# Kernel optimization log

Hardware: AMD Instinct MI355X
Metric: run time of the kernel (lower is better)

## Reference

```python
import jax, jax.numpy as jnp
import numpy as np
from jax import lax

B, T, U, V, D, H = 4, 256, 64, 1024, 256, 256
BLANK = V - 1
NEG = -1.0e30
CTC_W = 0.3


def setup_inputs():
    ks = jax.random.split(jax.random.key(0), 9)
    return {
        "x_enc": jax.random.normal(ks[0], (B, T, D), jnp.float32),
        "x_dec": jax.random.normal(ks[1], (B, U + 1, H), jnp.float32),
        "W_enc": jax.random.normal(ks[2], (D, H), jnp.float32) / float(np.sqrt(D)),
        "b_enc": jnp.zeros((H,), jnp.float32),
        "W_dec": jax.random.normal(ks[3], (H, H), jnp.float32) / float(np.sqrt(H)),
        "b_dec": jnp.zeros((H,), jnp.float32),
        "W_out": jax.random.normal(ks[4], (H, V), jnp.float32) / float(np.sqrt(H)),
        "b_out": jnp.zeros((V,), jnp.float32),
        "W_ctc": jax.random.normal(ks[5], (D, V), jnp.float32) / float(np.sqrt(D)),
        "b_ctc": jnp.zeros((V,), jnp.float32),
        "target": jax.random.randint(ks[6], (B, U), 0, V - 1, jnp.int32),
        "frame_length": (T - jax.random.randint(ks[7], (B,), 0, T // 4)).astype(jnp.int32),
        "target_length": (U - jax.random.randint(ks[8], (B,), 0, U // 4)).astype(jnp.int32),
    }


def _forward(x_enc, x_dec, W_enc, b_enc, W_dec, b_dec, W_out, b_out, W_ctc, b_ctc,
             target, frame_length, target_length):
    b_idx = jnp.arange(B)
    ft, tl = frame_length, target_length

    # ---- Joiner: broadcast-add of projected enc/pred states, tanh, output proj ----
    h = jnp.tanh((x_enc @ W_enc + b_enc)[:, :, None, :]
                 + (x_dec @ W_dec + b_dec)[:, None, :, :])        # [B,T,U+1,H]
    logp = jax.nn.log_softmax(h @ W_out + b_out, axis=-1)          # [B,T,U+1,V]

    # gather=True trick: only blank and target-label log-probs are needed
    lp_blank = logp[..., BLANK]                                    # [B,T,U+1]
    lp_label = jnp.take_along_axis(
        logp[:, :, :U, :],
        jnp.broadcast_to(target[:, None, :, None], (B, T, U, 1)), axis=3)[..., 0]  # [B,T,U]

    # ---- RNNT forward DP over the (T, U+1) lattice ----
    def u_scan(b0, lbl):
        # b0[u] = alpha[t-1,u] + blank[t-1,u]; alpha[t,u] = logaddexp(b0[u], alpha[t,u-1]+lbl[u-1])
        def step(c, xs):
            bu, lu = xs
            new = jnp.logaddexp(bu, c + lu)
            return new, new
        _, outs = lax.scan(step, b0[:, 0],
                           (jnp.moveaxis(b0[:, 1:], 1, 0), jnp.moveaxis(lbl, 1, 0)))
        return jnp.concatenate([b0[:, :1], jnp.moveaxis(outs, 0, 1)], axis=1)

    alpha0 = jnp.concatenate([jnp.zeros((B, 1), logp.dtype),
                              jnp.cumsum(lp_label[:, 0, :], axis=1)], axis=1)  # [B,U+1]

    def t_step(prev, xs):
        blk_prev, lbl_t = xs
        a = u_scan(prev + blk_prev, lbl_t)
        return a, a

    _, rest = lax.scan(t_step, alpha0,
                       (jnp.moveaxis(lp_blank[:, :-1, :], 1, 0),
                        jnp.moveaxis(lp_label[:, 1:, :], 1, 0)))
    alphas = jnp.concatenate([alpha0[None], rest], axis=0)          # [T,B,U+1]
    ll = alphas[ft - 1, b_idx, tl] + lp_blank[b_idx, ft - 1, tl]
    rnnt_loss = jnp.mean(-ll)

    # ---- CTC branch: linear head on encoder output + standard CTC DP ----
    logp_ctc = jax.nn.log_softmax(x_enc @ W_ctc + b_ctc, axis=-1)   # [B,T,V]
    S = 2 * U + 1
    ext = jnp.full((B, S), BLANK, jnp.int32).at[:, 1::2].set(target)
    emit = jnp.take_along_axis(logp_ctc,
                               jnp.broadcast_to(ext[:, None, :], (B, T, S)), axis=2)  # [B,T,S]
    skip = jnp.concatenate([jnp.zeros((B, 2), bool),
                            (ext[:, 2:] != BLANK) & (ext[:, 2:] != ext[:, :-2])], axis=1)
    c0 = jnp.full((B, S), NEG, logp_ctc.dtype).at[:, 0].set(emit[:, 0, 0]).at[:, 1].set(emit[:, 0, 1])

    def c_step(prev, xs):
        emit_t, t = xs
        p2 = jnp.concatenate([jnp.full((B, 1), NEG, prev.dtype), prev[:, :-1]], axis=1)
        p3 = jnp.where(skip,
                       jnp.concatenate([jnp.full((B, 2), NEG, prev.dtype), prev[:, :-2]], axis=1),
                       NEG)
        new = emit_t + jnp.logaddexp(jnp.logaddexp(prev, p2), p3)
        new = jnp.where((t < ft)[:, None], new, prev)  # freeze past frame_length
        return new, None

    cT, _ = lax.scan(c_step, c0, (jnp.moveaxis(emit[:, 1:, :], 1, 0), jnp.arange(1, T)))
    s_last = 2 * tl
    ll_ctc = jnp.logaddexp(cT[b_idx, s_last], cT[b_idx, s_last - 1])
    ctc_loss = jnp.where(ll_ctc < NEG / 2, 0.0, -ll_ctc).sum() / B  # zero_infinity, sum/B

    return rnnt_loss + CTC_W * ctc_loss


def reference(x_enc, x_dec, W_enc, b_enc, W_dec, b_dec, W_out, b_out, W_ctc, b_ctc,
              target, frame_length, target_length):
    return _forward(x_enc, x_dec, W_enc, b_enc, W_dec, b_dec, W_out, b_out, W_ctc, b_ctc,
                    target, frame_length, target_length)
```

## Files before the change

kernel.cpp:

```cpp
#include <hip/hip_runtime.h>
#include <hip/hip_bf16.h>

#define Bn 4
#define Tn 256
#define Un 64
#define UP1 65
#define Vn 1024
#define Dn 256
#define Hn 256
#define BLANKC 1023
#define NEGF (-1.0e30f)
#define CTCW 0.3f
#define R2E 1.4426950408889634f
#define LN2 0.6931471805599453f

typedef __attribute__((ext_vector_type(8))) short short8;
typedef __attribute__((ext_vector_type(4))) float f32x4;
typedef __attribute__((ext_vector_type(4))) unsigned int u32x4;

static __device__ __forceinline__ unsigned short f2bf(float f) {
  unsigned int u = __float_as_uint(f);
  u += 0x7FFFu + ((u >> 16) & 1u);
  return (unsigned short)(u >> 16);
}
static __device__ __forceinline__ unsigned int pack2bf(float a, float b) {
  return (unsigned int)f2bf(a) | ((unsigned int)f2bf(b) << 16);
}
static __device__ __forceinline__ float ftanh(float x) {
  float e = __expf(2.0f * x);
  return 1.0f - 2.0f / (e + 1.0f);
}
static __device__ __forceinline__ float ex2(float x) {
  return __builtin_amdgcn_exp2f(x);
}
static __device__ __forceinline__ float lg2(float x) {
  return __builtin_amdgcn_logf(x);
}
static __device__ __forceinline__ float laddexp2_(float x, float y) {
  float m = fmaxf(x, y);
  float d = y - x;
  return m + lg2(1.0f + ex2(-fabsf(d)));
}
static __device__ __forceinline__ float laddexp3_2(float a, float b, float c) {
  float m = fmaxf(fmaxf(a, b), c);
  return m + lg2(ex2(a - m) + ex2(b - m) + ex2(c - m));
}
static __device__ __forceinline__ float shfl_up1(float x) {
  int r = __builtin_amdgcn_update_dpp(0, __float_as_int(x), 0x138, 0xF, 0xF, false);
  return __int_as_float(r);
}

__global__ __launch_bounds__(256) void k_prep(
    const float* __restrict__ W_enc, const float* __restrict__ W_dec,
    const float* __restrict__ W_out, const float* __restrict__ W_ctc,
    unsigned short* __restrict__ Wt_enc, unsigned short* __restrict__ Wt_dec,
    unsigned short* __restrict__ Wt_out, unsigned short* __restrict__ Wt_ctc,
    float* __restrict__ out) {
  const int blk = blockIdx.x, tid = threadIdx.x;
  if (blk == 0 && tid == 0) out[0] = 0.0f;
  __shared__ float tilebuf[64][65];
  if (blk < 128) {
    const float* Wsrc = (blk < 64) ? W_out : W_ctc;
    unsigned short* Wd = (blk < 64) ? Wt_out : Wt_ctc;
    const int tt = blk & 63;
    const int k0 = (tt & 3) * 64, v0 = (tt >> 2) * 64;
#pragma unroll
    for (int rep = 0; rep < 16; ++rep) {
      int e = rep * 256 + tid;
      int rr = e >> 6, cc = e & 63;
      tilebuf[rr][cc] = Wsrc[(k0 + rr) * 1024 + (v0 + cc)];
    }
    __syncthreads();
#pragma unroll
    for (int rep = 0; rep < 16; ++rep) {
      int e = rep * 256 + tid;
      int nn = e >> 6, kk = e & 63;
      int n = v0 + nn, k = k0 + kk;
      int c = n >> 8, col = n & 255;
      int ks = k >> 5, sub = (k >> 3) & 3, k7 = k & 7;
      Wd[(c * 8 + ks) * 8192 + sub * 2048 + col * 8 + k7] = f2bf(tilebuf[kk][nn]);
    }
  } else {
    const float* Wsrc = (blk < 144) ? W_enc : W_dec;
    unsigned short* Wd = (blk < 144) ? Wt_enc : Wt_dec;
    const int tt = (blk - 128) & 15;
    const int k0 = (tt & 3) * 64, v0 = (tt >> 2) * 64;
#pragma unroll
    for (int rep = 0; rep < 16; ++rep) {
      int e = rep * 256 + tid;
      int rr = e >> 6, cc = e & 63;
      tilebuf[rr][cc] = Wsrc[(k0 + rr) * 256 + (v0 + cc)];
    }
    __syncthreads();
#pragma unroll
    for (int rep = 0; rep < 16; ++rep) {
      int e = rep * 256 + tid;
      int rr = e >> 6, cc = e & 63;
      Wd[(v0 + rr) * 256 + (k0 + cc)] = f2bf(tilebuf[cc][rr]);
    }
  }
}

__global__ __launch_bounds__(256) void k_lin(
    const float* __restrict__ x_enc, const float* __restrict__ x_dec,
    const unsigned short* __restrict__ Wt_enc, const float* __restrict__ b_enc,
    const unsigned short* __restrict__ Wt_dec, const float* __restrict__ b_dec,
    float* __restrict__ enc_lin, float* __restrict__ dec_lin) {
  __shared__ __align__(16) char Asw[64 * 512];
  const int tid = threadIdx.x;
  const int w = tid >> 6, l = tid & 63;
  const int l15 = l & 15, l4 = l >> 4;
  const bool enc = blockIdx.x < 16;
  const int m0 = enc ? blockIdx.x * 64 : (blockIdx.x - 16) * 64;
  const int Mlim = enc ? 1024 : 260;
  const float* xp = enc ? x_enc : x_dec;
  const unsigned short* Wt = enc ? Wt_enc : Wt_dec;
  const float* bias = enc ? b_enc : b_dec;
  float* outp = enc ? enc_lin : dec_lin;

#pragma unroll
  for (int it = 0; it < 8; ++it) {
    int e = (it << 8) + tid;
    int i = e >> 5;
    int k0 = (e & 31) << 3;
    int r = m0 + i;
    if (r > Mlim - 1) r = Mlim - 1;
    const float* sp = xp + r * 256 + k0;
    f32x4 e0 = *(const f32x4*)sp;
    f32x4 e1 = *(const f32x4*)(sp + 4);
    u32x4 pv;
    pv[0] = pack2bf(e0[0], e0[1]);
    pv[1] = pack2bf(e0[2], e0[3]);
    pv[2] = pack2bf(e1[0], e1[1]);
    pv[3] = pack2bf(e1[2], e1[3]);
    int byt = (i << 9) + (k0 << 1);
    byt ^= (i & 7) << 4;
    *(u32x4*)(Asw + byt) = pv;
  }
  __syncthreads();

  const int nb = w * 64;
  f32x4 acc[4][4] = {};
#pragma unroll
  for (int ks = 0; ks < 8; ++ks) {
    int k = ks * 32 + l4 * 8;
    short8 af[4];
#pragma unroll
    for (int mt = 0; mt < 4; ++mt) {
      int i = mt * 16 + l15;
      int byt = (i << 9) + (k << 1);
      byt ^= (i & 7) << 4;
      af[mt] = *(const short8*)(Asw + byt);
    }
    short8 bfr[4];
#pragma unroll
    for (int nt = 0; nt < 4; ++nt) {
      int n = nb + nt * 16 + l15;
      bfr[nt] = *(const short8*)(Wt + n * 256 + k);
    }
#pragma unroll
    for (int mt = 0; mt < 4; ++mt)
#pragma unroll
      for (int nt = 0; nt < 4; ++nt)
        acc[mt][nt] = __builtin_amdgcn_mfma_f32_16x16x32_bf16(
            af[mt], bfr[nt], acc[mt][nt], 0, 0, 0);
  }
  float biasv[4];
#pragma unroll
  for (int nt = 0; nt < 4; ++nt) biasv[nt] = bias[nb + nt * 16 + l15];
#pragma unroll
  for (int mt = 0; mt < 4; ++mt)
#pragma unroll
    for (int rr = 0; rr < 4; ++rr) {
      int row = m0 + mt * 16 + l4 * 4 + rr;
      if (row < Mlim) {
#pragma unroll
        for (int nt = 0; nt < 4; ++nt)
          outp[row * 256 + nb + nt * 16 + l15] = acc[mt][nt][rr] + biasv[nt];
      }
    }
}

__global__ __launch_bounds__(256) void k_join2(
    const float* __restrict__ enc_lin, const float* __restrict__ dec_lin,
    const unsigned short* __restrict__ Wt_out, const float* __restrict__ b_out,
    const float* __restrict__ x_enc,
    const unsigned short* __restrict__ Wt_ctc, const float* __restrict__ b_ctc,
    const int* __restrict__ target,
    float* __restrict__ lp_blank, float* __restrict__ lp_label,
    float* __restrict__ ctc_blank, float* __restrict__ ctc_lse,
    float* __restrict__ ctc_lab) {
  __shared__ __align__(16) char Asw[64 * 512];
  __shared__ float s_psum[4][64];
  __shared__ float s_blank[64], s_label[64];
  __shared__ int s_tgt[64];

  const int tid = threadIdx.x;
  const int w = tid >> 6, l = tid & 63;
  const int l15 = l & 15, l4 = l >> 4;

  const bool joiner = blockIdx.x >= 16;
  const unsigned short* Wt = joiner ? Wt_out : Wt_ctc;
  const float* bias = joiner ? b_out : b_ctc;

  const unsigned short* tb = Wt + l4 * 2048 + (w * 64 + l15) * 8;

  short8 bE[4], bO[4];
#define LOADB(REG, S)                                                          \
  {                                                                            \
    const unsigned short* p_ = tb + (S)*8192;                                  \
    _Pragma("unroll") for (int nt = 0; nt < 4; ++nt)                           \
        REG[nt] = *(const short8*)(p_ + nt * 128);                             \
  }
  LOADB(bE, 0)
  LOADB(bO, 1)

  int b, r0 = 0, g0 = 0;
  if (joiner) {
    const int bid = blockIdx.x - 16;
    b = bid / 260;
    r0 = (bid % 260) * 64;
#pragma unroll
    for (int it = 0; it < 8; ++it) {
      int e = (it << 8) + tid;
      int i = e >> 5;
      int k0 = (e & 31) << 3;
      int r = r0 + i;
      int t = r / 65;
      int u = r - t * 65;
      const float* ep = enc_lin + ((b * Tn + t) * Hn + k0);
      const float* dp = dec_lin + ((b * UP1 + u) * Hn + k0);
      f32x4 e0 = *(const f32x4*)ep;
      f32x4 e1 = *(const f32x4*)(ep + 4);
      f32x4 d0 = *(const f32x4*)dp;
      f32x4 d1 = *(const f32x4*)(dp + 4);
      u32x4 pv;
      pv[0] = pack2bf(ftanh(e0[0] + d0[0]), ftanh(e0[1] + d0[1]));
      pv[1] = pack2bf(ftanh(e0[2] + d0[2]), ftanh(e0[3] + d0[3]));
      pv[2] = pack2bf(ftanh(e1[0] + d1[0]), ftanh(e1[1] + d1[1]));
      pv[3] = pack2bf(ftanh(e1[2] + d1[2]), ftanh(e1[3] + d1[3]));
      int byt = (i << 9) + (k0 << 1);
      byt ^= (i & 7) << 4;
      *(u32x4*)(Asw + byt) = pv;
    }
    if (tid < 64) {
      int u = (r0 + tid) % 65;
      s_tgt[tid] = (u < Un) ? target[b * Un + u] : -1;
    }
  } else {
    g0 = blockIdx.x * 64;
    b = g0 >> 8;
#pragma unroll
    for (int it = 0; it < 8; ++it) {
      int e = (it << 8) + tid;
      int i = e >> 5;
      int k0 = (e & 31) << 3;
      const float* sp = x_enc + (g0 + i) * Dn + k0;
      f32x4 e0 = *(const f32x4*)sp;
      f32x4 e1 = *(const f32x4*)(sp + 4);
      u32x4 pv;
      pv[0] = pack2bf(e0[0], e0[1]);
      pv[1] = pack2bf(e0[2], e0[3]);
      pv[2] = pack2bf(e1[0], e1[1]);
      pv[3] = pack2bf(e1[2], e1[3]);
      int byt = (i << 9) + (k0 << 1);
      byt ^= (i & 7) << 4;
      *(u32x4*)(Asw + byt) = pv;
    }
    if (tid < 64) s_tgt[tid] = target[b * Un + tid];
  }
  __syncthreads();

  float ssum[16];
#pragma unroll
  for (int j = 0; j < 16; ++j) ssum[j] = 0.0f;

#define MFMASTEP(REG, KS)                                                      \
  {                                                                            \
    const int k_ = (KS)*32 + l4 * 8;                                           \
    _Pragma("unroll") for (int mt = 0; mt < 4; ++mt) {                         \
      int i_ = mt * 16 + l15;                                                  \
      int byt_ = ((i_ << 9) + (k_ << 1)) ^ ((i_ & 7) << 4);                    \
      short8 af_ = *(const short8*)(Asw + byt_);                               \
      _Pragma("unroll") for (int nt = 0; nt < 4; ++nt)                         \
          acc[mt][nt] = __builtin_amdgcn_mfma_f32_16x16x32_bf16(               \
              af_, REG[nt], acc[mt][nt], 0, 0, 0);                             \
    }                                                                          \
  }

#pragma unroll 1
  for (int c = 0; c < 4; ++c) {
    f32x4 acc[4][4] = {};
#pragma unroll
    for (int ks = 0; ks < 8; ks += 2) {
      const int s = c * 8 + ks;
      MFMASTEP(bE, ks)
      LOADB(bE, (s + 2 < 32) ? s + 2 : 31)
      __builtin_amdgcn_sched_barrier(0);
      MFMASTEP(bO, ks + 1)
      LOADB(bO, (s + 3 < 32) ? s + 3 : 31)
      __builtin_amdgcn_sched_barrier(0);
    }
    const int nb = c * 256 + w * 64;
    float biasv[4];
#pragma unroll
    for (int nt = 0; nt < 4; ++nt) biasv[nt] = bias[nb + nt * 16 + l15];
#pragma unroll
    for (int mt = 0; mt < 4; ++mt)
#pragma unroll
      for (int nt = 0; nt < 4; ++nt)
#pragma unroll
        for (int rr = 0; rr < 4; ++rr) acc[mt][nt][rr] += biasv[nt];

    if (joiner) {
      if (c == 3 && w == 3 && l15 == 15) {
#pragma unroll
        for (int mt = 0; mt < 4; ++mt)
#pragma unroll
          for (int rr = 0; rr < 4; ++rr)
            s_blank[mt * 16 + l4 * 4 + rr] = acc[mt][3][rr];
      }
#pragma unroll
      for (int mt = 0; mt < 4; ++mt)
#pragma unroll
        for (int rr = 0; rr < 4; ++rr) {
          int row = mt * 16 + l4 * 4 + rr;
          int tg = s_tgt[row];
          if ((tg >> 8) == c && ((tg >> 6) & 3) == w && (tg & 15) == l15) {
            int ntv = (tg >> 4) & 3;
            float v01 = (ntv & 1) ? acc[mt][1][rr] : acc[mt][0][rr];
            float v23 = (ntv & 1) ? acc[mt][3][rr] : acc[mt][2][rr];
            s_label[row] = (ntv & 2) ? v23 : v01;
          }
        }
    } else {
      if (c == 3 && w == 3 && l15 == 15) {
#pragma unroll
        for (int mt = 0; mt < 4; ++mt)
#pragma unroll
          for (int rr = 0; rr < 4; ++rr)
            s_blank[mt * 16 + l4 * 4 + rr] = acc[mt][3][rr];
      }
#pragma unroll 1
      for (int u = 0; u < 64; ++u) {
        int tgu = s_tgt[u];
        if ((tgu >> 8) == c && ((tgu >> 6) & 3) == w) {
          int ntv = (tgu >> 4) & 3;
          if ((tgu & 15) == l15) {
#pragma unroll
            for (int mt = 0; mt < 4; ++mt)
#pragma unroll
              for (int rr = 0; rr < 4; ++rr) {
                float v01 = (ntv & 1) ? acc[mt][1][rr] : acc[mt][0][rr];
                float v23 = (ntv & 1) ? acc[mt][3][rr] : acc[mt][2][rr];
                float v = (ntv & 2) ? v23 : v01;
                ctc_lab[(g0 + mt * 16 + l4 * 4 + rr) * 64 + u] = v;
              }
          }
        }
      }
    }
#pragma unroll
    for (int mt = 0; mt < 4; ++mt)
#pragma unroll
      for (int rr = 0; rr < 4; ++rr)
        ssum[mt * 4 + rr] += __expf(acc[mt][0][rr]) + __expf(acc[mt][1][rr]) +
                             __expf(acc[mt][2][rr]) + __expf(acc[mt][3][rr]);
  }
#undef MFMASTEP
#undef LOADB

#pragma unroll
  for (int ms = 1; ms < 16; ms <<= 1)
#pragma unroll
    for (int j = 0; j < 16; ++j) ssum[j] += __shfl_xor(ssum[j], ms, 64);
  if (l15 == 0) {
#pragma unroll
    for (int j = 0; j < 16; ++j)
      s_psum[w][(j >> 2) * 16 + l4 * 4 + (j & 3)] = ssum[j];
  }
  __syncthreads();

  if (tid < 64) {
    float tot = s_psum[0][tid] + s_psum[1][tid] + s_psum[2][tid] + s_psum[3][tid];
    float lse = __logf(tot);
    if (joiner) {
      int r = r0 + tid;
      int t = r / 65;
      int u = r - t * 65;
      lp_blank[(b * Tn + t) * UP1 + u] = s_blank[tid] - lse;
      if (u < Un) lp_label[(b * Tn + t) * Un + u] = s_label[tid] - lse;
    } else {
      ctc_blank[g0 + tid] = s_blank[tid] - lse;
      ctc_lse[g0 + tid] = lse;
    }
  }
}

__global__ __launch_bounds__(256) void k_dp(
    const float* __restrict__ lp_blank, const float* __restrict__ lp_label,
    const float* __restrict__ ctc_blank, const float* __restrict__ ctc_lse,
    const float* __restrict__ ctc_lab,
    const int* __restrict__ target,
    const int* __restrict__ flen, const int* __restrict__ tlen,
    float* __restrict__ out) {
  __shared__ float sA[256 * 66];
  __shared__ __align__(16) float sB[16384];
  __shared__ float sC[256], sD[256];
  __shared__ float cT[129];
  const int tid = threadIdx.x;
  const int l = tid & 63;

  if (blockIdx.x < 4) {
    const int b = blockIdx.x;
    for (int i = tid; i < 16640; i += 256) {
      int r = i / 65, cidx = i - r * 65;
      sA[r * 66 + cidx] = lp_blank[b * 16640 + i] * R2E;
    }
    for (int i = tid; i < 16384; i += 256) sB[i] = lp_label[b * 16384 + i] * R2E;
    __syncthreads();
    if (tid < 64) {
      const int ft = flen[b], tl = tlen[b];
      const int dstar = ft - 1 + tl;
      const bool isown = (l == tl);
      const bool is64 = (tl == 64) && (l == 63);
      const int lc = (l >= 1) ? l - 1 : 0;

#define RLOAD(D0, VB, VL, VB64, VL64)                                          \
  _Pragma("unroll") for (int j = 0; j < 8; ++j) {                              \
    const int d_ = (D0) + j;                                                   \
    const int t_ = d_ - l;                                                     \
    const int tbc_ = (t_ < 1) ? 1 : (t_ > 255 ? 255 : t_);                     \
    const int tcc_ = (t_ < 0) ? 0 : (t_ > 255 ? 255 : t_);                     \
    VB[j] = sA[(tbc_ - 1) * 66 + l];                                           \
    VL[j] = (l == 0) ? NEGF : sB[tcc_ * 64 + lc];                              \
    const int t64_ = d_ - 64;                                                  \
    const int t64b_ = (t64_ < 1) ? 1 : (t64_ > 255 ? 255 : t64_);              \
    const int t64c_ = (t64_ < 0) ? 0 : (t64_ > 255 ? 255 : t64_);              \
    VB64[j] = sA[(t64b_ - 1) * 66 + 64];                                       \
    VL64[j] = sB[t64c_ * 64 + 63];                                             \
  }

      float cvb[8], cvl[8], cvb64[8], cvl64[8];
      RLOAD(1, cvb, cvl, cvb64, cvl64);
      float a = (l == 0) ? 0.0f : NEGF;
      float a64 = NEGF, cap = NEGF;
      for (int d0 = 1; d0 <= 313; d0 += 8) {
        float nvb[8], nvl[8], nvb64[8], nvl64[8];
        RLOAD(d0 + 8, nvb, nvl, nvb64, nvl64);
        __builtin_amdgcn_sched_barrier(0);
#pragma unroll
        for (int j = 0; j < 8; ++j) {
          const int d = d0 + j;
          float aleft = shfl_up1(a);
          float x = a + cvb[j];
          float y = aleft + cvl[j];
          float nw = laddexp2_(x, y);
          float nw64 = laddexp2_(a64 + cvb64[j], a + cvl64[j]);
          a = nw;
          a64 = (l == 63) ? nw64 : a64;
          bool hit = (d == dstar);
          cap = (hit && isown) ? a : cap;
          cap = (hit && is64) ? a64 : cap;
        }
        __builtin_amdgcn_sched_barrier(0);
#pragma unroll
        for (int j = 0; j < 8; ++j) {
          cvb[j] = nvb[j];
          cvl[j] = nvl[j];
          cvb64[j] = nvb64[j];
          cvl64[j] = nvl64[j];
        }
      }
#undef RLOAD
      bool owner = (tl < 64) ? isown : (l == 63);
      if (owner)
        atomicAdd(out, -0.25f * LN2 * (cap + sA[(ft - 1) * 66 + tl]));
    }
  } else {
    const int b = blockIdx.x - 4;
    for (int i = tid; i < 16384; i += 256) sB[i] = ctc_lab[b * 16384 + i] * R2E;
    sC[tid] = ctc_blank[b * 256 + tid] * R2E;
    sD[tid] = ctc_lse[b * 256 + tid] * R2E;
    __syncthreads();
    if (tid < 64) {
      const int ft = flen[b], tl = tlen[b];
      const int tg = target[b * Un + l];
      const int tgp = (l >= 1) ? target[b * Un + l - 1] : -1;
      const bool skip1 = (l >= 1) && (tg != tgp);

#define CLOAD(T0, EB, E1)                                                      \
  _Pragma("unroll") for (int j = 0; j < 8; ++j) {                              \
    const int tc_ = ((T0) + j > 255) ? 255 : (T0) + j;                         \
    EB[j] = sC[tc_];                                                           \
    E1[j] = sB[tc_ * 64 + l] - sD[tc_];                                        \
  }

      float ceb[8], ce1[8];
      CLOAD(1, ceb, ce1);
      float a0 = (l == 0) ? sC[0] : NEGF;
      float a1 = (l == 0) ? (sB[0] - sD[0]) : NEGF;
      float a2 = NEGF;
      for (int t0 = 1; t0 <= 249; t0 += 8) {
        float neb[8], ne1[8];
        CLOAD(t0 + 8, neb, ne1);
        __builtin_amdgcn_sched_barrier(0);
#pragma unroll
        for (int j = 0; j < 8; ++j) {
          const int t = t0 + j;
          float pm1 = shfl_up1(a1);
          pm1 = (l == 0) ? NEGF : pm1;
          float n0 = ceb[j] + laddexp2_(a0, pm1);
          float n1 = ce1[j] + laddexp3_2(a1, a0, skip1 ? pm1 : NEGF);
          float n2 = ceb[j] + laddexp2_(a2, a1);
          bool run = (t < ft);
          a0 = run ? n0 : a0;
          a1 = run ? n1 : a1;
          a2 = (run && (l == 63)) ? n2 : a2;
        }
        __builtin_amdgcn_sched_barrier(0);
#pragma unroll
        for (int j = 0; j < 8; ++j) {
          ceb[j] = neb[j];
          ce1[j] = ne1[j];
        }
      }
#undef CLOAD
      cT[2 * l] = a0;
      cT[2 * l + 1] = a1;
      if (l == 63) cT[128] = a2;
      __builtin_amdgcn_s_waitcnt(0);
      if (l == 0) {
        int sl = 2 * tl;
        float ll = laddexp2_(cT[sl], cT[sl - 1]);
        float lb = (ll < NEGF * 0.5f * R2E) ? 0.0f : -ll;
        atomicAdd(out, CTCW * 0.25f * LN2 * lb);
      }
    }
  }
}

extern "C" void kernel_launch(void* const* d_in, const int* in_sizes, int n_in,
                              void* d_out, int out_size, void* d_ws, size_t ws_size,
                              hipStream_t stream) {
  (void)in_sizes; (void)n_in; (void)out_size; (void)ws_size;
  const float* x_enc = (const float*)d_in[0];
  const float* x_dec = (const float*)d_in[1];
  const float* W_enc = (const float*)d_in[2];
  const float* b_enc = (const float*)d_in[3];
  const float* W_dec = (const float*)d_in[4];
  const float* b_dec = (const float*)d_in[5];
  const float* W_out = (const float*)d_in[6];
  const float* b_out = (const float*)d_in[7];
  const float* W_ctc = (const float*)d_in[8];
  const float* b_ctc = (const float*)d_in[9];
  const int* target = (const int*)d_in[10];
  const int* flen = (const int*)d_in[11];
  const int* tlen = (const int*)d_in[12];

  float* ws = (float*)d_ws;
  float* enc_lin = ws;
  float* dec_lin = ws + 262144;
  float* lp_blank = ws + 328704;
  float* lp_label = ws + 395264;
  float* ctc_blank = ws + 460800;
  float* ctc_lse = ws + 461824;
  float* ctc_lab = ws + 462848;
  unsigned short* Wt_out = (unsigned short*)(ws + 528384);
  unsigned short* Wt_ctc = Wt_out + 262144;
  unsigned short* Wt_enc = (unsigned short*)lp_blank;
  unsigned short* Wt_dec = (unsigned short*)lp_label;
  float* out = (float*)d_out;

  k_prep<<<dim3(160), dim3(256), 0, stream>>>(
      W_enc, W_dec, W_out, W_ctc, Wt_enc, Wt_dec, Wt_out, Wt_ctc, out);
  k_lin<<<dim3(21), dim3(256), 0, stream>>>(
      x_enc, x_dec, Wt_enc, b_enc, Wt_dec, b_dec, enc_lin, dec_lin);
  k_join2<<<dim3(1056), dim3(256), 0, stream>>>(
      enc_lin, dec_lin, Wt_out, b_out, x_enc, Wt_ctc, b_ctc, target,
      lp_blank, lp_label, ctc_blank, ctc_lse, ctc_lab);
  k_dp<<<dim3(8), dim3(64 * 4), 0, stream>>>(
      lp_blank, lp_label, ctc_blank, ctc_lse, ctc_lab, target, flen, tlen, out);
}
```

Measured before the change: 122.6 us.

## Deepen B-operand prefetch, stagger column chunks per block, work in base-2 logits

The joiner/CTC GEMM kernel now keeps four B-fragment register buffers instead of two, and each block starts its column-chunk sweep at a different offset (bid&3), so the L2 load on the shared weight matrix is spread across chunks. Activations and bias are pre-scaled by log2(e), which lets the softmax use exp2/log2 directly and removes the R2E multiplies in the DP kernels. The DP loaders also become vectorized float4 copies. The costs are higher register pressure from the extra buffers and a changed CTC infinity threshold constant.

```diff
diff --git a/kernel.cpp b/kernel.cpp
--- a/kernel.cpp
+++ b/kernel.cpp
@@ -198,28 +198,34 @@
   const int tid = threadIdx.x;
   const int w = tid >> 6, l = tid & 63;
   const int l15 = l & 15, l4 = l >> 4;
-
-  const bool joiner = blockIdx.x >= 16;
+  const int bid = blockIdx.x;
+
+  const bool joiner = bid >= 16;
   const unsigned short* Wt = joiner ? Wt_out : Wt_ctc;
   const float* bias = joiner ? b_out : b_ctc;
 
   const unsigned short* tb = Wt + l4 * 2048 + (w * 64 + l15) * 8;
 
-  short8 bE[4], bO[4];
+  short8 b0[4], b1[4], b2[4], b3[4];
 #define LOADB(REG, S)                                                          \
   {                                                                            \
     const unsigned short* p_ = tb + (S)*8192;                                  \
     _Pragma("unroll") for (int nt = 0; nt < 4; ++nt)                           \
         REG[nt] = *(const short8*)(p_ + nt * 128);                             \
   }
-  LOADB(bE, 0)
-  LOADB(bO, 1)
+  {
+    const int cc0 = bid & 3;
+    LOADB(b0, cc0 * 8 + 0)
+    LOADB(b1, cc0 * 8 + 1)
+    LOADB(b2, cc0 * 8 + 2)
+    LOADB(b3, cc0 * 8 + 3)
+  }
 
   int b, r0 = 0, g0 = 0;
   if (joiner) {
-    const int bid = blockIdx.x - 16;
-    b = bid / 260;
-    r0 = (bid % 260) * 64;
+    const int jbid = bid - 16;
+    b = jbid / 260;
+    r0 = (jbid % 260) * 64;
 #pragma unroll
     for (int it = 0; it < 8; ++it) {
       int e = (it << 8) + tid;
@@ -235,10 +241,10 @@
       f32x4 d0 = *(const f32x4*)dp;
       f32x4 d1 = *(const f32x4*)(dp + 4);
       u32x4 pv;
-      pv[0] = pack2bf(ftanh(e0[0] + d0[0]), ftanh(e0[1] + d0[1]));
-      pv[1] = pack2bf(ftanh(e0[2] + d0[2]), ftanh(e0[3] + d0[3]));
-      pv[2] = pack2bf(ftanh(e1[0] + d1[0]), ftanh(e1[1] + d1[1]));
-      pv[3] = pack2bf(ftanh(e1[2] + d1[2]), ftanh(e1[3] + d1[3]));
+      pv[0] = pack2bf(ftanh(e0[0] + d0[0]) * R2E, ftanh(e0[1] + d0[1]) * R2E);
+      pv[1] = pack2bf(ftanh(e0[2] + d0[2]) * R2E, ftanh(e0[3] + d0[3]) * R2E);
+      pv[2] = pack2bf(ftanh(e1[0] + d1[0]) * R2E, ftanh(e1[1] + d1[1]) * R2E);
+      pv[3] = pack2bf(ftanh(e1[2] + d1[2]) * R2E, ftanh(e1[3] + d1[3]) * R2E);
       int byt = (i << 9) + (k0 << 1);
       byt ^= (i & 7) << 4;
       *(u32x4*)(Asw + byt) = pv;
@@ -248,7 +254,7 @@
       s_tgt[tid] = (u < Un) ? target[b * Un + u] : -1;
     }
   } else {
-    g0 = blockIdx.x * 64;
+    g0 = bid * 64;
     b = g0 >> 8;
 #pragma unroll
     for (int it = 0; it < 8; ++it) {
@@ -259,10 +265,10 @@
       f32x4 e0 = *(const f32x4*)sp;
       f32x4 e1 = *(const f32x4*)(sp + 4);
       u32x4 pv;
-      pv[0] = pack2bf(e0[0], e0[1]);
-      pv[1] = pack2bf(e0[2], e0[3]);
-      pv[2] = pack2bf(e1[0], e1[1]);
-      pv[3] = pack2bf(e1[2], e1[3]);
+      pv[0] = pack2bf(e0[0] * R2E, e0[1] * R2E);
+      pv[1] = pack2bf(e0[2] * R2E, e0[3] * R2E);
+      pv[2] = pack2bf(e1[0] * R2E, e1[1] * R2E);
+      pv[3] = pack2bf(e1[2] * R2E, e1[3] * R2E);
       int byt = (i << 9) + (k0 << 1);
       byt ^= (i & 7) << 4;
       *(u32x4*)(Asw + byt) = pv;
@@ -287,24 +293,31 @@
               af_, REG[nt], acc[mt][nt], 0, 0, 0);                             \
     }                                                                          \
   }
+#define SB __builtin_amdgcn_sched_barrier(0)
 
 #pragma unroll 1
-  for (int c = 0; c < 4; ++c) {
+  for (int cr = 0; cr < 4; ++cr) {
+    const int cc = (cr + bid) & 3;
+    const int ccn = (cr + 1 + bid) & 3;
+    const int sc = cc * 8;
+    const int rn0 = (cr < 3) ? ccn * 8 + 0 : sc + 4;
+    const int rn1 = (cr < 3) ? ccn * 8 + 1 : sc + 5;
+    const int rn2 = (cr < 3) ? ccn * 8 + 2 : sc + 6;
+    const int rn3 = (cr < 3) ? ccn * 8 + 3 : sc + 7;
     f32x4 acc[4][4] = {};
-#pragma unroll
-    for (int ks = 0; ks < 8; ks += 2) {
-      const int s = c * 8 + ks;
-      MFMASTEP(bE, ks)
-      LOADB(bE, (s + 2 < 32) ? s + 2 : 31)
-      __builtin_amdgcn_sched_barrier(0);
-      MFMASTEP(bO, ks + 1)
-      LOADB(bO, (s + 3 < 32) ? s + 3 : 31)
-      __builtin_amdgcn_sched_barrier(0);
-    }
-    const int nb = c * 256 + w * 64;
+    MFMASTEP(b0, 0) LOADB(b0, sc + 4) SB;
+    MFMASTEP(b1, 1) LOADB(b1, sc + 5) SB;
+    MFMASTEP(b2, 2) LOADB(b2, sc + 6) SB;
+    MFMASTEP(b3, 3) LOADB(b3, sc + 7) SB;
+    MFMASTEP(b0, 4) LOADB(b0, rn0) SB;
+    MFMASTEP(b1, 5) LOADB(b1, rn1) SB;
+    MFMASTEP(b2, 6) LOADB(b2, rn2) SB;
+    MFMASTEP(b3, 7) LOADB(b3, rn3) SB;
+
+    const int nb = cc * 256 + w * 64;
     float biasv[4];
 #pragma unroll
-    for (int nt = 0; nt < 4; ++nt) biasv[nt] = bias[nb + nt * 16 + l15];
+    for (int nt = 0; nt < 4; ++nt) biasv[nt] = bias[nb + nt * 16 + l15] * R2E;
 #pragma unroll
     for (int mt = 0; mt < 4; ++mt)
 #pragma unroll
@@ -313,7 +326,7 @@
         for (int rr = 0; rr < 4; ++rr) acc[mt][nt][rr] += biasv[nt];
 
     if (joiner) {
-      if (c == 3 && w == 3 && l15 == 15) {
+      if (cc == 3 && w == 3 && l15 == 15) {
 #pragma unroll
         for (int mt = 0; mt < 4; ++mt)
 #pragma unroll
@@ -326,7 +339,7 @@
         for (int rr = 0; rr < 4; ++rr) {
           int row = mt * 16 + l4 * 4 + rr;
           int tg = s_tgt[row];
-          if ((tg >> 8) == c && ((tg >> 6) & 3) == w && (tg & 15) == l15) {
+          if ((tg >> 8) == cc && ((tg >> 6) & 3) == w && (tg & 15) == l15) {
             int ntv = (tg >> 4) & 3;
             float v01 = (ntv & 1) ? acc[mt][1][rr] : acc[mt][0][rr];
             float v23 = (ntv & 1) ? acc[mt][3][rr] : acc[mt][2][rr];
@@ -334,7 +347,7 @@
           }
         }
     } else {
-      if (c == 3 && w == 3 && l15 == 15) {
+      if (cc == 3 && w == 3 && l15 == 15) {
 #pragma unroll
         for (int mt = 0; mt < 4; ++mt)
 #pragma unroll
@@ -344,7 +357,7 @@
 #pragma unroll 1
       for (int u = 0; u < 64; ++u) {
         int tgu = s_tgt[u];
-        if ((tgu >> 8) == c && ((tgu >> 6) & 3) == w) {
+        if ((tgu >> 8) == cc && ((tgu >> 6) & 3) == w) {
           int ntv = (tgu >> 4) & 3;
           if ((tgu & 15) == l15) {
 #pragma unroll
@@ -364,11 +377,12 @@
     for (int mt = 0; mt < 4; ++mt)
 #pragma unroll
       for (int rr = 0; rr < 4; ++rr)
-        ssum[mt * 4 + rr] += __expf(acc[mt][0][rr]) + __expf(acc[mt][1][rr]) +
-                             __expf(acc[mt][2][rr]) + __expf(acc[mt][3][rr]);
+        ssum[mt * 4 + rr] += ex2(acc[mt][0][rr]) + ex2(acc[mt][1][rr]) +
+                             ex2(acc[mt][2][rr]) + ex2(acc[mt][3][rr]);
   }
 #undef MFMASTEP
 #undef LOADB
+#undef SB
 
 #pragma unroll
   for (int ms = 1; ms < 16; ms <<= 1)
@@ -383,7 +397,7 @@
 
   if (tid < 64) {
     float tot = s_psum[0][tid] + s_psum[1][tid] + s_psum[2][tid] + s_psum[3][tid];
-    float lse = __logf(tot);
+    float lse = lg2(tot);
     if (joiner) {
       int r = r0 + tid;
       int t = r / 65;
@@ -415,9 +429,13 @@
     const int b = blockIdx.x;
     for (int i = tid; i < 16640; i += 256) {
       int r = i / 65, cidx = i - r * 65;
-      sA[r * 66 + cidx] = lp_blank[b * 16640 + i] * R2E;
-    }
-    for (int i = tid; i < 16384; i += 256) sB[i] = lp_label[b * 16384 + i] * R2E;
+      sA[r * 66 + cidx] = lp_blank[b * 16640 + i];
+    }
+    {
+      const f32x4* g2 = (const f32x4*)(lp_label + b * 16384);
+      f32x4* s2 = (f32x4*)sB;
+      for (int i = tid; i < 4096; i += 256) s2[i] = g2[i];
+    }
     __syncthreads();
     if (tid < 64) {
       const int ft = flen[b], tl = tlen[b];
@@ -479,9 +497,13 @@
     }
   } else {
     const int b = blockIdx.x - 4;
-    for (int i = tid; i < 16384; i += 256) sB[i] = ctc_lab[b * 16384 + i] * R2E;
-    sC[tid] = ctc_blank[b * 256 + tid] * R2E;
-    sD[tid] = ctc_lse[b * 256 + tid] * R2E;
+    {
+      const f32x4* g2 = (const f32x4*)(ctc_lab + b * 16384);
+      f32x4* s2 = (f32x4*)sB;
+      for (int i = tid; i < 4096; i += 256) s2[i] = g2[i];
+      sC[tid] = ctc_blank[b * 256 + tid];
+      sD[tid] = ctc_lse[b * 256 + tid];
+    }
     __syncthreads();
     if (tid < 64) {
       const int ft = flen[b], tl = tlen[b];
@@ -533,7 +555,7 @@
       if (l == 0) {
         int sl = 2 * tl;
         float ll = laddexp2_(cT[sl], cT[sl - 1]);
-        float lb = (ll < NEGF * 0.5f * R2E) ? 0.0f : -ll;
+        float lb = (ll < NEGF * 0.7f) ? 0.0f : -ll;
         atomicAdd(out, CTCW * 0.25f * LN2 * lb);
       }
     }
```

Result: slower. 148.4 us (+21.1%).
